# Kernel optimization log

Measured on AMD Instinct MI355X. Metric: run time of the kernel, lower is better.

## Reference

```python
import jax, jax.numpy as jnp
import numpy as np

S, A, F, D = 512, 128, 128, 6


def setup_inputs() -> dict:
    key = jax.random.key(0)
    k1, k2 = jax.random.split(key)
    atoms = jax.random.normal(k1, (S, A, F), dtype=jnp.float32)
    # edges in [-1, A); -1 marks missing neighbors (padding)
    edges = jax.random.randint(k2, (S, A, D), -1, A, dtype=jnp.int64)
    return {"atoms": atoms, "edges": edges}


def lookup_neighbors(atoms, edges, maskvalue, include_self):
    # atoms: (S, A, F), edges: (S, A, D) with -1 padding
    s, a, f = atoms.shape
    # prepend a masked "null atom" row at index 0; shift edge indices by +1
    null_row = jnp.full((s, 1, f), maskvalue, dtype=atoms.dtype)
    masked_atoms = jnp.concatenate([null_row, atoms], axis=1)  # (S, A+1, F)
    idx = edges + 1  # -1 padding -> 0 (null row)
    if include_self:
        self_idx = jnp.broadcast_to(jnp.arange(1, a + 1, dtype=idx.dtype)[None, :, None], (s, a, 1))
        idx = jnp.concatenate([self_idx, idx], axis=-1)  # (S, A, D+1)
    # gather neighbor features: (S, A, D+1, F)
    batch_idx = jnp.arange(s)[:, None, None]
    return masked_atoms[batch_idx, idx]


def reference(atoms, edges):
    neighbor_feats = lookup_neighbors(atoms, edges, maskvalue=-jnp.inf, include_self=True)
    max_features = neighbor_feats.max(axis=2)  # (S, A, F)
    atom_degrees = (edges != -1).sum(axis=-1, keepdims=True)  # (S, A, 1)
    general_atom_mask = (atom_degrees != 0).astype(atoms.dtype)
    return max_features * general_atom_mask
```

## Files before the change

### kernel.cpp

```cpp
#include <hip/hip_runtime.h>
#include <stdint.h>


constexpr int S  = 512;
constexpr int A  = 128;
constexpr int F  = 128;
constexpr int D  = 6;
constexpr int QF = 32;
constexpr int ROWB = QF * 4;

#define GLOBAL_AS __attribute__((address_space(1)))
#define LDS_AS    __attribute__((address_space(3)))

__global__ __launch_bounds__(256, 8) void graphpool_kernel(
    const float* __restrict__ atoms,
    const int*   __restrict__ edges,
    float*       __restrict__ out)
{
    __shared__ __align__(16) float sl[A * QF];
    __shared__ __align__(16) int   se[A * 8];

    const int tid  = threadIdx.x;
    const int qb   = blockIdx.x & 3;
    const int s    = blockIdx.x >> 2;
    const int wave = tid >> 6;
    const int lane = tid & 63;

    const float* slab = atoms + (size_t)s * (A * F) + qb * QF;
    {
        const int rowq = lane >> 3;
        const int colq = lane & 7;
#pragma unroll
        for (int i = 0; i < 4; ++i) {
            const int chunk = wave * 4 + i;
            const float* gp = slab + (size_t)(chunk * 8 + rowq) * F + colq * 4;
            float* lp = &sl[chunk * 256];
            __builtin_amdgcn_global_load_lds((const GLOBAL_AS float*)gp,
                                             (LDS_AS float*)lp, 16, 0, 0);
        }
    }

    if (tid < A) {
        const int* eg = edges + ((size_t)s * A + tid) * D;
        const int i0 = eg[0], i1 = eg[1], i2 = eg[2];
        const int i3 = eg[3], i4 = eg[4], i5 = eg[5];
        const int deg = (i0 >= 0) + (i1 >= 0) + (i2 >= 0) +
                        (i3 >= 0) + (i4 >= 0) + (i5 >= 0);
        const int self = tid * ROWB;
        int4 w0, w1;
        w0.x = (i0 >= 0) ? i0 * ROWB : self;
        w0.y = (i1 >= 0) ? i1 * ROWB : self;
        w0.z = (i2 >= 0) ? i2 * ROWB : self;
        w0.w = (i3 >= 0) ? i3 * ROWB : self;
        w1.x = (i4 >= 0) ? i4 * ROWB : self;
        w1.y = (i5 >= 0) ? i5 * ROWB : self;
        w1.z = __float_as_int(deg ? 1.0f : 0.0f);
        w1.w = 0;
        *(int4*)&se[tid * 8]     = w0;
        *(int4*)&se[tid * 8 + 4] = w1;
    }

    __syncthreads();

    const int q    = tid & 7;
    const int qoff = q * 16;
    const char* lbase = (const char*)sl;
    float* outb = out + (size_t)s * (A * F) + qb * QF + q * 4;

#pragma unroll
    for (int p = 0; p < 4; ++p) {
        const int a = p * 32 + (tid >> 3);

        const int4 e0 = *(const int4*)&se[a * 8];
        const int4 e1 = *(const int4*)&se[a * 8 + 4];
        const float maskf = __int_as_float(e1.z);

        float4 m = *(const float4*)(lbase + a * ROWB + qoff);
        float4 v;
        v = *(const float4*)(lbase + e0.x + qoff);
        m.x = fmaxf(m.x, v.x); m.y = fmaxf(m.y, v.y);
        m.z = fmaxf(m.z, v.z); m.w = fmaxf(m.w, v.w);
        v = *(const float4*)(lbase + e0.y + qoff);
        m.x = fmaxf(m.x, v.x); m.y = fmaxf(m.y, v.y);
        m.z = fmaxf(m.z, v.z); m.w = fmaxf(m.w, v.w);
        v = *(const float4*)(lbase + e0.z + qoff);
        m.x = fmaxf(m.x, v.x); m.y = fmaxf(m.y, v.y);
        m.z = fmaxf(m.z, v.z); m.w = fmaxf(m.w, v.w);
        v = *(const float4*)(lbase + e0.w + qoff);
        m.x = fmaxf(m.x, v.x); m.y = fmaxf(m.y, v.y);
        m.z = fmaxf(m.z, v.z); m.w = fmaxf(m.w, v.w);
        v = *(const float4*)(lbase + e1.x + qoff);
        m.x = fmaxf(m.x, v.x); m.y = fmaxf(m.y, v.y);
        m.z = fmaxf(m.z, v.z); m.w = fmaxf(m.w, v.w);
        v = *(const float4*)(lbase + e1.y + qoff);
        m.x = fmaxf(m.x, v.x); m.y = fmaxf(m.y, v.y);
        m.z = fmaxf(m.z, v.z); m.w = fmaxf(m.w, v.w);

        m.x *= maskf; m.y *= maskf; m.z *= maskf; m.w *= maskf;

        *(float4*)(outb + (size_t)a * F) = m;
    }
}

extern "C" void kernel_launch(void* const* d_in, const int* in_sizes, int n_in,
                              void* d_out, int out_size, void* d_ws, size_t ws_size,
                              hipStream_t stream) {
    const float* atoms = (const float*)d_in[0];
    const int*   edges = (const int*)d_in[1];
    float*       out   = (float*)d_out;

    graphpool_kernel<<<S * 4, 256, 0, stream>>>(atoms, edges, out);
}
```

Before: 83.11 us.

## Process two feature quarters per block with register-prefetched second slab

Each block now handles two 32-feature quarter slabs instead of one, halving the grid and reusing the decoded edge table across both. The second slab is loaded into registers while the first quarter's gather runs, then written to LDS for the second pass. This amortizes edge decoding and overlaps global loads with LDS gather work. In exchange it doubles shared memory per block, lowers the occupancy bound from 8 to 4, and adds a second barrier.

```diff
diff --git a/kernel.cpp b/kernel.cpp
--- a/kernel.cpp
+++ b/kernel.cpp
@@ -1,5 +1,4 @@
 #include <hip/hip_runtime.h>
-#include <stdint.h>
 
 
 constexpr int S  = 512;
@@ -8,64 +7,19 @@
 constexpr int D  = 6;
 constexpr int QF = 32;
 constexpr int ROWB = QF * 4;
+constexpr int SLOT = A * QF;
 
 #define GLOBAL_AS __attribute__((address_space(1)))
 #define LDS_AS    __attribute__((address_space(3)))
 
-__global__ __launch_bounds__(256, 8) void graphpool_kernel(
-    const float* __restrict__ atoms,
-    const int*   __restrict__ edges,
-    float*       __restrict__ out)
+__device__ __forceinline__ void gather_unit(const float* __restrict__ sl_slab,
+                                            const int*   __restrict__ se,
+                                            float* __restrict__ outb,
+                                            int tid)
 {
-    __shared__ __align__(16) float sl[A * QF];
-    __shared__ __align__(16) int   se[A * 8];
-
-    const int tid  = threadIdx.x;
-    const int qb   = blockIdx.x & 3;
-    const int s    = blockIdx.x >> 2;
-    const int wave = tid >> 6;
-    const int lane = tid & 63;
-
-    const float* slab = atoms + (size_t)s * (A * F) + qb * QF;
-    {
-        const int rowq = lane >> 3;
-        const int colq = lane & 7;
-#pragma unroll
-        for (int i = 0; i < 4; ++i) {
-            const int chunk = wave * 4 + i;
-            const float* gp = slab + (size_t)(chunk * 8 + rowq) * F + colq * 4;
-            float* lp = &sl[chunk * 256];
-            __builtin_amdgcn_global_load_lds((const GLOBAL_AS float*)gp,
-                                             (LDS_AS float*)lp, 16, 0, 0);
-        }
-    }
-
-    if (tid < A) {
-        const int* eg = edges + ((size_t)s * A + tid) * D;
-        const int i0 = eg[0], i1 = eg[1], i2 = eg[2];
-        const int i3 = eg[3], i4 = eg[4], i5 = eg[5];
-        const int deg = (i0 >= 0) + (i1 >= 0) + (i2 >= 0) +
-                        (i3 >= 0) + (i4 >= 0) + (i5 >= 0);
-        const int self = tid * ROWB;
-        int4 w0, w1;
-        w0.x = (i0 >= 0) ? i0 * ROWB : self;
-        w0.y = (i1 >= 0) ? i1 * ROWB : self;
-        w0.z = (i2 >= 0) ? i2 * ROWB : self;
-        w0.w = (i3 >= 0) ? i3 * ROWB : self;
-        w1.x = (i4 >= 0) ? i4 * ROWB : self;
-        w1.y = (i5 >= 0) ? i5 * ROWB : self;
-        w1.z = __float_as_int(deg ? 1.0f : 0.0f);
-        w1.w = 0;
-        *(int4*)&se[tid * 8]     = w0;
-        *(int4*)&se[tid * 8 + 4] = w1;
-    }
-
-    __syncthreads();
-
     const int q    = tid & 7;
     const int qoff = q * 16;
-    const char* lbase = (const char*)sl;
-    float* outb = out + (size_t)s * (A * F) + qb * QF + q * 4;
+    const char* lbase = (const char*)sl_slab;
 
 #pragma unroll
     for (int p = 0; p < 4; ++p) {
@@ -102,6 +56,78 @@
     }
 }
 
+__global__ __launch_bounds__(256, 4) void graphpool_kernel(
+    const float* __restrict__ atoms,
+    const int*   __restrict__ edges,
+    float*       __restrict__ out)
+{
+    __shared__ __align__(16) float sl[2 * SLOT];
+    __shared__ __align__(16) int   se[A * 8];
+
+    const int tid  = threadIdx.x;
+    const int h    = blockIdx.x & 1;
+    const int s    = blockIdx.x >> 1;
+    const int wave = tid >> 6;
+    const int lane = tid & 63;
+
+    const float* slab0 = atoms + (size_t)s * (A * F) + (h * 2) * QF;
+    const float* slab1 = slab0 + QF;
+
+    {
+        const int rowq = lane >> 3;
+        const int colq = lane & 7;
+#pragma unroll
+        for (int i = 0; i < 4; ++i) {
+            const int chunk = wave * 4 + i;
+            const float* gp = slab0 + (size_t)(chunk * 8 + rowq) * F + colq * 4;
+            float* lp = &sl[chunk * 256];
+            __builtin_amdgcn_global_load_lds((const GLOBAL_AS float*)gp,
+                                             (LDS_AS float*)lp, 16, 0, 0);
+        }
+    }
+    if (tid < A) {
+        const int* eg = edges + ((size_t)s * A + tid) * D;
+        const int i0 = eg[0], i1 = eg[1], i2 = eg[2];
+        const int i3 = eg[3], i4 = eg[4], i5 = eg[5];
+        const int deg = (i0 >= 0) + (i1 >= 0) + (i2 >= 0) +
+                        (i3 >= 0) + (i4 >= 0) + (i5 >= 0);
+        const int self = tid * ROWB;
+        int4 w0, w1;
+        w0.x = (i0 >= 0) ? i0 * ROWB : self;
+        w0.y = (i1 >= 0) ? i1 * ROWB : self;
+        w0.z = (i2 >= 0) ? i2 * ROWB : self;
+        w0.w = (i3 >= 0) ? i3 * ROWB : self;
+        w1.x = (i4 >= 0) ? i4 * ROWB : self;
+        w1.y = (i5 >= 0) ? i5 * ROWB : self;
+        w1.z = __float_as_int(deg ? 1.0f : 0.0f);
+        w1.w = 0;
+        *(int4*)&se[tid * 8]     = w0;
+        *(int4*)&se[tid * 8 + 4] = w1;
+    }
+
+    __syncthreads();
+
+    const int prow = tid >> 3;
+    const int pcol = (tid & 7) * 4;
+    float4 r0 = *(const float4*)(slab1 + (size_t)(prow +  0) * F + pcol);
+    float4 r1 = *(const float4*)(slab1 + (size_t)(prow + 32) * F + pcol);
+    float4 r2 = *(const float4*)(slab1 + (size_t)(prow + 64) * F + pcol);
+    float4 r3 = *(const float4*)(slab1 + (size_t)(prow + 96) * F + pcol);
+
+    float* outb0 = out + (size_t)s * (A * F) + (h * 2) * QF + (tid & 7) * 4;
+    gather_unit(sl, se, outb0, tid);
+
+    *(float4*)(&sl[SLOT + (tid +   0) * 4]) = r0;
+    *(float4*)(&sl[SLOT + (tid + 256) * 4]) = r1;
+    *(float4*)(&sl[SLOT + (tid + 512) * 4]) = r2;
+    *(float4*)(&sl[SLOT + (tid + 768) * 4]) = r3;
+
+    __syncthreads();
+
+    float* outb1 = outb0 + QF;
+    gather_unit(sl + SLOT, se, outb1, tid);
+}
+
 extern "C" void kernel_launch(void* const* d_in, const int* in_sizes, int n_in,
                               void* d_out, int out_size, void* d_ws, size_t ws_size,
                               hipStream_t stream) {
@@ -109,5 +135,5 @@
     const int*   edges = (const int*)d_in[1];
     float*       out   = (float*)d_out;
 
-    graphpool_kernel<<<S * 4, 256, 0, stream>>>(atoms, edges, out);
+    graphpool_kernel<<<S * 2, 256, 0, stream>>>(atoms, edges, out);
 }
```

New measurement: 84.22 us. About the same (+1.3%).
